# Kernel tuning notes

Measured on AMD Instinct MI355X. Metric: run time of the kernel, lower is better.

## Reference

```python
import jax, jax.numpy as jnp
import numpy as np

EPS_LN = 1e-5


def layer_norm(x, g, b):
    mu = jnp.mean(x, axis=-1, keepdims=True)
    var = jnp.mean((x - mu) ** 2, axis=-1, keepdims=True)
    return (x - mu) * jax.lax.rsqrt(var + EPS_LN) * g + b


def setup_inputs() -> dict:
    key = jax.random.key(0)
    ks = jax.random.split(key, 16)
    N, E, H, EA = 25000, 400000, 128, 1
    h = jax.random.normal(ks[0], (N, H), dtype=jnp.float32)
    coord = jax.random.normal(ks[1], (N, 3), dtype=jnp.float32)
    edge_index = jax.random.randint(ks[2], (2, E), 0, N, dtype=jnp.int64)
    edge_attr = jax.random.normal(ks[3], (E, EA), dtype=jnp.float32)

    def lin(k, fan_in, fan_out):
        lim = 1.0 / np.sqrt(fan_in)
        return jax.random.uniform(k, (fan_in, fan_out), jnp.float32, -lim, lim)

    in_edge = 2 * H + 1 + EA  # 258
    params = {
        'e_W1': lin(ks[4], in_edge, H), 'e_b1': jnp.zeros((H,), jnp.float32),
        'e_g1': jnp.ones((H,), jnp.float32), 'e_be1': jnp.zeros((H,), jnp.float32),
        'e_W2': lin(ks[5], H, H), 'e_b2': jnp.zeros((H,), jnp.float32),
        'e_g2': jnp.ones((H,), jnp.float32), 'e_be2': jnp.zeros((H,), jnp.float32),
        'n_W1': lin(ks[6], 2 * H, H), 'n_b1': jnp.zeros((H,), jnp.float32),
        'n_g1': jnp.ones((H,), jnp.float32), 'n_be1': jnp.zeros((H,), jnp.float32),
        'n_W2': lin(ks[7], H, H), 'n_b2': jnp.zeros((H,), jnp.float32),
        'c_W1': lin(ks[8], H, H), 'c_b1': jnp.zeros((H,), jnp.float32),
        'c_g1': jnp.ones((H,), jnp.float32), 'c_be1': jnp.zeros((H,), jnp.float32),
        # xavier_uniform with gain=0.001, no bias
        'c_W2': jax.random.uniform(ks[9], (H, 1), jnp.float32, -1.0, 1.0) * (0.001 * np.sqrt(6.0 / (H + 1))),
    }
    return dict(h=h, edge_index=edge_index, coord=coord, edge_attr=edge_attr, **params)


def reference(h, edge_index, coord, edge_attr,
              e_W1, e_b1, e_g1, e_be1, e_W2, e_b2, e_g2, e_be2,
              n_W1, n_b1, n_g1, n_be1, n_W2, n_b2,
              c_W1, c_b1, c_g1, c_be1, c_W2):
    N = h.shape[0]
    row, col = edge_index[0], edge_index[1]

    coord_diff = coord[row] - coord[col]                     # [E,3]
    radial = jnp.sum(coord_diff ** 2, axis=1, keepdims=True)  # [E,1]
    norm = jnp.sqrt(radial + 1e-8)
    coord_diff = coord_diff / (norm + 1.0)

    inp = jnp.concatenate([h[row], h[col], radial, edge_attr], axis=1)  # [E,258]
    x = jax.nn.silu(layer_norm(inp @ e_W1 + e_b1, e_g1, e_be1))
    edge_feat = jax.nn.silu(layer_norm(x @ e_W2 + e_b2, e_g2, e_be2))   # [E,H]

    cm = jax.nn.silu(layer_norm(edge_feat @ c_W1 + c_b1, c_g1, c_be1)) @ c_W2  # [E,1]
    trans = coord_diff * cm                                   # [E,3]

    coord_out = coord + jax.ops.segment_sum(trans, row, num_segments=N)
    agg = jax.ops.segment_sum(edge_feat, row, num_segments=N)  # [N,H]

    node_in = jnp.concatenate([h, agg], axis=1)               # [N,2H]
    out = jax.nn.silu(layer_norm(node_in @ n_W1 + n_b1, n_g1, n_be1)) @ n_W2 + n_b2
    out = h + out  # recurrent
    return out, coord_out
```

## Files before the change

### kernel.cpp

```cpp
#include <hip/hip_runtime.h>
#include <math.h>

#define H 128
#define KE 256
#define KN 256
#define XSTR 136

typedef __attribute__((ext_vector_type(8))) short bf16x8;
typedef __attribute__((ext_vector_type(4))) float f32x4;

__device__ __forceinline__ float silu_f(float x) { return x / (1.0f + __expf(-x)); }

__device__ __forceinline__ unsigned short f2bf(float f) {
    unsigned int u = __float_as_uint(f);
    unsigned int r = u + 0x7FFFu + ((u >> 16) & 1u);
    return (unsigned short)(r >> 16);
}

__device__ __forceinline__ unsigned int pkbf(float a, float b) {
#if defined(__has_builtin)
#if __has_builtin(__builtin_amdgcn_cvt_pk_bf16_f32)
    typedef __attribute__((ext_vector_type(2))) __bf16 bf16x2_t;
    bf16x2_t v = __builtin_amdgcn_cvt_pk_bf16_f32(a, b);
    return *(unsigned int*)&v;
#else
    return (unsigned int)f2bf(a) | ((unsigned int)f2bf(b) << 16);
#endif
#else
    return (unsigned int)f2bf(a) | ((unsigned int)f2bf(b) << 16);
#endif
}

__device__ __forceinline__ void atomic_pk_add_bf16(unsigned short* addr, unsigned int pkv) {
    asm volatile("global_atomic_pk_add_bf16 %0, %1, off"
                 :: "v"(addr), "v"(pkv) : "memory");
}

template<int CTRL>
__device__ __forceinline__ float dpp_add(float x) {
    int t = __builtin_amdgcn_update_dpp(0, __float_as_int(x), CTRL, 0xF, 0xF, true);
    return x + __int_as_float(t);
}
__device__ __forceinline__ float red16(float x) {
    x = dpp_add<0x128>(x);
    x = dpp_add<0x124>(x);
    x = dpp_add<0x122>(x);
    x = dpp_add<0x121>(x);
    return x;
}

__device__ __forceinline__ void wfrag(const float* __restrict__ W,
                                      unsigned short* __restrict__ Wf, int f) {
    int kb = f >> 9, rem = f & 511;
    int nt = rem >> 6, lane = rem & 63;
    int quad = lane >> 4, l15 = lane & 15;
    int n = nt * 16 + l15, k0 = kb * 32 + quad * 8;
    union { bf16x8 v; unsigned short u[8]; } pk;
    #pragma unroll
    for (int j = 0; j < 8; ++j) pk.u[j] = f2bf(W[(size_t)(k0 + j) * H + n]);
    *(bf16x8*)&Wf[(size_t)f * 8] = pk.v;
}

__global__ __launch_bounds__(256) void prep_all(
    const float* __restrict__ h, unsigned short* __restrict__ hb, int n4_h,
    float* __restrict__ aggz, int n4_agg,
    const float* __restrict__ coord, float* __restrict__ coord_out, int n_coord,
    const float* __restrict__ eW1, const float* __restrict__ eW2,
    const float* __restrict__ cW1, const float* __restrict__ nW1,
    const float* __restrict__ nW2,
    unsigned short* __restrict__ eW1f, unsigned short* __restrict__ eW2f,
    unsigned short* __restrict__ cW1f, unsigned short* __restrict__ nW1f,
    unsigned short* __restrict__ nW2f,
    int b0, int b1, int b2)
{
    int b = blockIdx.x;
    int t = threadIdx.x;
    if (b < b0) {
        int i = b * 256 + t;
        if (i < n4_h) {
            float4 f = ((const float4*)h)[i];
            ((uint2*)hb)[i] = make_uint2(pkbf(f.x, f.y), pkbf(f.z, f.w));
        }
    } else if (b < b1) {
        int i = (b - b0) * 256 + t;
        if (i < n4_agg) ((float4*)aggz)[i] = (float4){0.f, 0.f, 0.f, 0.f};
    } else if (b < b2) {
        int i = (b - b1) * 256 + t;
        if (i < n_coord) coord_out[i] = coord[i];
    } else {
        int idx = (b - b2) * 256 + t;
        if      (idx <  4096) wfrag(eW1, eW1f, idx);
        else if (idx <  8192) wfrag(nW1, nW1f, idx - 4096);
        else if (idx < 10240) wfrag(eW2, eW2f, idx - 8192);
        else if (idx < 12288) wfrag(cW1, cW1f, idx - 10240);
        else if (idx < 14336) wfrag(nW2, nW2f, idx - 12288);
    }
}

__device__ __forceinline__ void ln_silu_store1(
    f32x4* acc, const float* __restrict__ bias, const float* __restrict__ g,
    const float* __restrict__ be, unsigned short* X, int l15, int quad)
{
    float s[4] = {0,0,0,0}, q[4] = {0,0,0,0};
    #pragma unroll
    for (int nt = 0; nt < 8; ++nt) {
        float b = bias[nt * 16 + l15];
        #pragma unroll
        for (int r = 0; r < 4; ++r) {
            float x = acc[nt][r] + b; acc[nt][r] = x; s[r] += x; q[r] += x * x;
        }
    }
    #pragma unroll
    for (int r = 0; r < 4; ++r) { s[r] = red16(s[r]); q[r] = red16(q[r]); }
    #pragma unroll
    for (int r = 0; r < 4; ++r) {
        float mu = s[r] * 0.0078125f, v = q[r] * 0.0078125f - mu * mu;
        s[r] = mu; q[r] = rsqrtf(v + 1e-5f);
    }
    #pragma unroll
    for (int nt = 0; nt < 8; ++nt) {
        float gg = g[nt * 16 + l15], bb = be[nt * 16 + l15];
        float y0 = silu_f(fmaf(acc[nt][0], q[0] * gg, bb - s[0] * (q[0] * gg)));
        float y1 = silu_f(fmaf(acc[nt][1], q[1] * gg, bb - s[1] * (q[1] * gg)));
        float y2 = silu_f(fmaf(acc[nt][2], q[2] * gg, bb - s[2] * (q[2] * gg)));
        float y3 = silu_f(fmaf(acc[nt][3], q[3] * gg, bb - s[3] * (q[3] * gg)));
        acc[nt][0] = y0; acc[nt][1] = y1; acc[nt][2] = y2; acc[nt][3] = y3;
        unsigned int p01 = pkbf(y0, y1), p23 = pkbf(y2, y3);
        const int col = nt * 16 + l15;
        X[(quad * 4 + 0) * XSTR + col] = (unsigned short)p01;
        X[(quad * 4 + 1) * XSTR + col] = (unsigned short)(p01 >> 16);
        X[(quad * 4 + 2) * XSTR + col] = (unsigned short)p23;
        X[(quad * 4 + 3) * XSTR + col] = (unsigned short)(p23 >> 16);
    }
}

__global__ __launch_bounds__(64, 4) void edge_kernel(
    const unsigned short* __restrict__ hb, const int* __restrict__ ei,
    const float* __restrict__ coord, const float* __restrict__ eattr,
    const unsigned short* __restrict__ eW1f, const float* __restrict__ eW1,
    const float* __restrict__ eb1, const float* __restrict__ eg1, const float* __restrict__ ebe1,
    const unsigned short* __restrict__ eW2f,
    const float* __restrict__ eb2, const float* __restrict__ eg2, const float* __restrict__ ebe2,
    const unsigned short* __restrict__ cW1f,
    const float* __restrict__ cb1, const float* __restrict__ cg1, const float* __restrict__ cbe1,
    const float* __restrict__ cW2,
    unsigned short* __restrict__ aggb, float* __restrict__ coord_out, int E)
{
    __shared__ unsigned short X[16 * XSTR];

    const int lane = threadIdx.x;
    const int l15 = lane & 15, quad = lane >> 4;
    const int ge0 = blockIdx.x * 16;

    int el  = ge0 + l15;
    int elc = (el < E) ? el : (E - 1);
    int rowl = ei[elc], coll = ei[E + elc];
    float dx = coord[rowl * 3 + 0] - coord[coll * 3 + 0];
    float dy = coord[rowl * 3 + 1] - coord[coll * 3 + 1];
    float dz = coord[rowl * 3 + 2] - coord[coll * 3 + 2];
    float radial = dx * dx + dy * dy + dz * dz;
    float inv = 1.0f / (sqrtf(radial + 1e-8f) + 1.0f);
    float cdx = dx * inv, cdy = dy * inv, cdz = dz * inv;
    float ea = eattr[elc];

    f32x4 acc[8];
    #pragma unroll
    for (int nt = 0; nt < 8; ++nt) acc[nt] = (f32x4){0.f, 0.f, 0.f, 0.f};

    for (int kb = 0; kb < 8; ++kb) {
        int ko = (kb & 3) * 32 + quad * 8;
        bf16x8 af = *(const bf16x8*)(hb + (size_t)((kb < 4) ? rowl : coll) * H + ko);
        const unsigned short* bp = eW1f + ((size_t)kb * 8) * 512 + (size_t)lane * 8;
        #pragma unroll
        for (int nt = 0; nt < 8; ++nt) {
            bf16x8 bf = *(const bf16x8*)(bp + (size_t)nt * 512);
            acc[nt] = __builtin_amdgcn_mfma_f32_16x16x32_bf16(af, bf, acc[nt], 0, 0, 0);
        }
    }

    {
        float rad_r[4], ea_r[4];
        #pragma unroll
        for (int r = 0; r < 4; ++r) {
            rad_r[r] = __shfl(radial, quad * 4 + r, 64);
            ea_r[r]  = __shfl(ea,     quad * 4 + r, 64);
        }
        #pragma unroll
        for (int nt = 0; nt < 8; ++nt) {
            float w256 = eW1[256 * H + nt * 16 + l15];
            float w257 = eW1[257 * H + nt * 16 + l15];
            #pragma unroll
            for (int r = 0; r < 4; ++r)
                acc[nt][r] += rad_r[r] * w256 + ea_r[r] * w257;
        }
    }

    ln_silu_store1(acc, eb1, eg1, ebe1, X, l15, quad);

    f32x4 ac2[8];
    #pragma unroll
    for (int nt = 0; nt < 8; ++nt) ac2[nt] = (f32x4){0.f, 0.f, 0.f, 0.f};
    for (int kb = 0; kb < 4; ++kb) {
        bf16x8 af = *(const bf16x8*)&X[l15 * XSTR + kb * 32 + quad * 8];
        const unsigned short* bp = eW2f + ((size_t)kb * 8) * 512 + (size_t)lane * 8;
        #pragma unroll
        for (int nt = 0; nt < 8; ++nt) {
            bf16x8 bf = *(const bf16x8*)(bp + (size_t)nt * 512);
            ac2[nt] = __builtin_amdgcn_mfma_f32_16x16x32_bf16(af, bf, ac2[nt], 0, 0, 0);
        }
    }

    ln_silu_store1(ac2, eb2, eg2, ebe2, X, l15, quad);

    {
        int rowm[4];
        #pragma unroll
        for (int r = 0; r < 4; ++r) rowm[r] = __shfl(rowl, quad * 4 + r, 64);
        #pragma unroll
        for (int c4 = 0; c4 < 4; ++c4) {
            #pragma unroll
            for (int r = 0; r < 4; ++r) {
                int geh = ge0 + quad * 4 + r;
                if (geh < E) {
                    unsigned int pkv =
                        *(const unsigned int*)&X[(quad * 4 + r) * XSTR + c4 * 32 + 2 * l15];
                    atomic_pk_add_bf16(aggb + (size_t)rowm[r] * H + c4 * 32 + 2 * l15, pkv);
                }
            }
        }
    }

    #pragma unroll
    for (int nt = 0; nt < 8; ++nt) acc[nt] = (f32x4){0.f, 0.f, 0.f, 0.f};
    for (int kb = 0; kb < 4; ++kb) {
        bf16x8 af = *(const bf16x8*)&X[l15 * XSTR + kb * 32 + quad * 8];
        const unsigned short* bp = cW1f + ((size_t)kb * 8) * 512 + (size_t)lane * 8;
        #pragma unroll
        for (int nt = 0; nt < 8; ++nt) {
            bf16x8 bf = *(const bf16x8*)(bp + (size_t)nt * 512);
            acc[nt] = __builtin_amdgcn_mfma_f32_16x16x32_bf16(af, bf, acc[nt], 0, 0, 0);
        }
    }

    {
        float s[4] = {0,0,0,0}, q[4] = {0,0,0,0};
        #pragma unroll
        for (int nt = 0; nt < 8; ++nt) {
            float b = cb1[nt * 16 + l15];
            #pragma unroll
            for (int r = 0; r < 4; ++r) {
                float x = acc[nt][r] + b; acc[nt][r] = x; s[r] += x; q[r] += x * x;
            }
        }
        #pragma unroll
        for (int r = 0; r < 4; ++r) { s[r] = red16(s[r]); q[r] = red16(q[r]); }
        #pragma unroll
        for (int r = 0; r < 4; ++r) {
            float mu = s[r] * 0.0078125f, v = q[r] * 0.0078125f - mu * mu;
            s[r] = mu; q[r] = rsqrtf(v + 1e-5f);
        }
        float cm[4] = {0,0,0,0};
        #pragma unroll
        for (int nt = 0; nt < 8; ++nt) {
            float gg = cg1[nt * 16 + l15], bb = cbe1[nt * 16 + l15];
            float w2 = cW2[nt * 16 + l15];
            #pragma unroll
            for (int r = 0; r < 4; ++r) {
                float a = q[r] * gg, c = bb - s[r] * a;
                cm[r] += silu_f(acc[nt][r] * a + c) * w2;
            }
        }
        #pragma unroll
        for (int r = 0; r < 4; ++r) cm[r] = red16(cm[r]);
        #pragma unroll
        for (int r = 0; r < 4; ++r) {
            int src = quad * 4 + r;
            float cdxr = __shfl(cdx, src, 64);
            float cdyr = __shfl(cdy, src, 64);
            float cdzr = __shfl(cdz, src, 64);
            int rw = __shfl(rowl, src, 64);
            float comp = (l15 == 0) ? cdxr : ((l15 == 1) ? cdyr : cdzr);
            int geh = ge0 + src;
            if (l15 < 3 && geh < E)
                atomicAdd(&coord_out[(size_t)rw * 3 + l15], comp * cm[r]);
        }
    }
}

__global__ __launch_bounds__(256, 4) void node_kernel(
    const unsigned short* __restrict__ hb, const float* __restrict__ h,
    const unsigned short* __restrict__ aggb,
    const unsigned short* __restrict__ nW1f,
    const float* __restrict__ nb1, const float* __restrict__ ng1, const float* __restrict__ nbe1,
    const unsigned short* __restrict__ nW2f, const float* __restrict__ nb2,
    float* __restrict__ out, int N)
{
    __shared__ unsigned short Xs[4][16 * XSTR];

    const int wv   = threadIdx.x >> 6;
    const int lane = threadIdx.x & 63;
    const int l15 = lane & 15, quad = lane >> 4;
    const int gn0 = (blockIdx.x * 4 + wv) * 16;
    unsigned short* X = &Xs[wv][0];

    if (gn0 >= N) return;
    int nl = gn0 + l15; if (nl >= N) nl = N - 1;

    f32x4 acc[8];
    #pragma unroll
    for (int nt = 0; nt < 8; ++nt) acc[nt] = (f32x4){0.f, 0.f, 0.f, 0.f};

    for (int kb = 0; kb < 8; ++kb) {
        int ko = (kb & 3) * 32 + quad * 8;
        const unsigned short* src = (kb < 4) ? hb : aggb;
        bf16x8 af = *(const bf16x8*)(src + (size_t)nl * H + ko);
        const unsigned short* bp = nW1f + ((size_t)kb * 8) * 512 + (size_t)lane * 8;
        #pragma unroll
        for (int nt = 0; nt < 8; ++nt) {
            bf16x8 bf = *(const bf16x8*)(bp + (size_t)nt * 512);
            acc[nt] = __builtin_amdgcn_mfma_f32_16x16x32_bf16(af, bf, acc[nt], 0, 0, 0);
        }
    }

    ln_silu_store1(acc, nb1, ng1, nbe1, X, l15, quad);

    f32x4 ac2[8];
    #pragma unroll
    for (int nt = 0; nt < 8; ++nt) ac2[nt] = (f32x4){0.f, 0.f, 0.f, 0.f};
    for (int kb = 0; kb < 4; ++kb) {
        bf16x8 af = *(const bf16x8*)&X[l15 * XSTR + kb * 32 + quad * 8];
        const unsigned short* bp = nW2f + ((size_t)kb * 8) * 512 + (size_t)lane * 8;
        #pragma unroll
        for (int nt = 0; nt < 8; ++nt) {
            bf16x8 bf = *(const bf16x8*)(bp + (size_t)nt * 512);
            ac2[nt] = __builtin_amdgcn_mfma_f32_16x16x32_bf16(af, bf, ac2[nt], 0, 0, 0);
        }
    }

    #pragma unroll
    for (int nt = 0; nt < 8; ++nt) {
        float b = nb2[nt * 16 + l15];
        #pragma unroll
        for (int r = 0; r < 4; ++r) {
            int gn = gn0 + quad * 4 + r;
            if (gn < N) {
                size_t idx = (size_t)gn * H + nt * 16 + l15;
                out[idx] = ac2[nt][r] + b + h[idx];
            }
        }
    }
}

extern "C" void kernel_launch(void* const* d_in, const int* in_sizes, int n_in,
                              void* d_out, int out_size, void* d_ws, size_t ws_size,
                              hipStream_t stream) {
    const float* h     = (const float*)d_in[0];
    const int*   ei    = (const int*)d_in[1];
    const float* coord = (const float*)d_in[2];
    const float* eattr = (const float*)d_in[3];
    const float* eW1   = (const float*)d_in[4];
    const float* eb1   = (const float*)d_in[5];
    const float* eg1   = (const float*)d_in[6];
    const float* ebe1  = (const float*)d_in[7];
    const float* eW2   = (const float*)d_in[8];
    const float* eb2   = (const float*)d_in[9];
    const float* eg2   = (const float*)d_in[10];
    const float* ebe2  = (const float*)d_in[11];
    const float* nW1   = (const float*)d_in[12];
    const float* nb1   = (const float*)d_in[13];
    const float* ng1   = (const float*)d_in[14];
    const float* nbe1  = (const float*)d_in[15];
    const float* nW2   = (const float*)d_in[16];
    const float* nb2   = (const float*)d_in[17];
    const float* cW1   = (const float*)d_in[18];
    const float* cb1   = (const float*)d_in[19];
    const float* cg1   = (const float*)d_in[20];
    const float* cbe1  = (const float*)d_in[21];
    const float* cW2   = (const float*)d_in[22];

    const int N = in_sizes[0] / H;
    const int E = in_sizes[1] / 2;

    float* out       = (float*)d_out;
    float* coord_out = out + (size_t)N * H;

    char* ws = (char*)d_ws;
    size_t o = 0;
    unsigned short* aggb = (unsigned short*)(ws + o); o += (size_t)N * H * 2;
    unsigned short* hb   = (unsigned short*)(ws + o); o += (size_t)N * H * 2;
    unsigned short* eW1f = (unsigned short*)(ws + o); o += (size_t)H * KE * 2;
    unsigned short* eW2f = (unsigned short*)(ws + o); o += (size_t)H * H * 2;
    unsigned short* cW1f = (unsigned short*)(ws + o); o += (size_t)H * H * 2;
    unsigned short* nW1f = (unsigned short*)(ws + o); o += (size_t)H * KN * 2;
    unsigned short* nW2f = (unsigned short*)(ws + o); o += (size_t)H * H * 2;

    const int n4_h   = N * H / 4;
    const int n4_agg = N * H / 8;
    const int n_co   = N * 3;
    const int b0 = (n4_h   + 255) / 256;
    const int b1 = b0 + (n4_agg + 255) / 256;
    const int b2 = b1 + (n_co   + 255) / 256;
    const int bw = (4096 + 4096 + 2048 + 2048 + 2048 + 255) / 256;
    prep_all<<<b2 + bw, 256, 0, stream>>>(
        h, hb, n4_h, (float*)aggb, n4_agg, coord, coord_out, n_co,
        eW1, eW2, cW1, nW1, nW2,
        eW1f, eW2f, cW1f, nW1f, nW2f, b0, b1, b2);

    edge_kernel<<<(E + 15) / 16, 64, 0, stream>>>(
        hb, ei, coord, eattr,
        eW1f, eW1, eb1, eg1, ebe1,
        eW2f, eb2, eg2, ebe2,
        cW1f, cb1, cg1, cbe1, cW2,
        aggb, coord_out, E);

    node_kernel<<<(N + 63) / 64, 256, 0, stream>>>(
        hb, h, aggb, nW1f, nb1, ng1, nbe1, nW2f, nb2, out, N);
}
```

Measured before the change: 337.2 us.

## Precompute per-node edge-MLP first-layer projections and gather them per edge

The first edge linear layer is linear in h[row] and h[col], so a new kernel computes h@W1_top and h@W1_bottom once per node (N rows instead of E) and stores them as bf16. The edge kernel then gathers the two 128-wide projections per edge, sums them into shared memory and adds the radial/edge_attr terms, replacing the K=256 MFMA loop. This removes most of the first-layer FLOPs at the cost of an extra launch, an N×256 bf16 workspace and an extra bf16 rounding of the projections, which changes numerics. The per-edge gather width stays at 512 bytes, the same as before.

```diff
diff --git a/kernel.cpp b/kernel.cpp
--- a/kernel.cpp
+++ b/kernel.cpp
@@ -5,6 +5,7 @@
 #define KE 256
 #define KN 256
 #define XSTR 136
+#define SSTR 132
 
 typedef __attribute__((ext_vector_type(8))) short bf16x8;
 typedef __attribute__((ext_vector_type(4))) float f32x4;
@@ -30,6 +31,9 @@
     return (unsigned int)f2bf(a) | ((unsigned int)f2bf(b) << 16);
 #endif
 }
+
+__device__ __forceinline__ float bflo(unsigned int w) { return __uint_as_float(w << 16); }
+__device__ __forceinline__ float bfhi(unsigned int w) { return __uint_as_float(w & 0xFFFF0000u); }
 
 __device__ __forceinline__ void atomic_pk_add_bf16(unsigned short* addr, unsigned int pkv) {
     asm volatile("global_atomic_pk_add_bf16 %0, %1, off"
@@ -97,6 +101,63 @@
     }
 }
 
+__global__ __launch_bounds__(256, 4) void proj_kernel(
+    const unsigned short* __restrict__ hb,
+    const unsigned short* __restrict__ eW1f,
+    unsigned short* __restrict__ Pb, int N)
+{
+    __shared__ unsigned short Ys[4][16 * 256];
+
+    const int wv = threadIdx.x >> 6;
+    const int lane = threadIdx.x & 63;
+    const int l15 = lane & 15, quad = lane >> 4;
+    const int gn0 = (blockIdx.x * 4 + wv) * 16;
+    unsigned short* Y = &Ys[wv][0];
+
+    if (gn0 >= N) return;
+    int nl = gn0 + l15; if (nl >= N) nl = N - 1;
+
+    f32x4 a1[8], a2[8];
+    #pragma unroll
+    for (int nt = 0; nt < 8; ++nt) {
+        a1[nt] = (f32x4){0.f, 0.f, 0.f, 0.f};
+        a2[nt] = (f32x4){0.f, 0.f, 0.f, 0.f};
+    }
+
+    for (int kb = 0; kb < 4; ++kb) {
+        int ko = kb * 32 + quad * 8;
+        bf16x8 af = *(const bf16x8*)(hb + (size_t)nl * H + ko);
+        const unsigned short* bp1 = eW1f + ((size_t)kb * 8) * 512 + (size_t)lane * 8;
+        const unsigned short* bp2 = eW1f + ((size_t)(kb + 4) * 8) * 512 + (size_t)lane * 8;
+        #pragma unroll
+        for (int nt = 0; nt < 8; ++nt) {
+            bf16x8 b1 = *(const bf16x8*)(bp1 + (size_t)nt * 512);
+            bf16x8 b2 = *(const bf16x8*)(bp2 + (size_t)nt * 512);
+            a1[nt] = __builtin_amdgcn_mfma_f32_16x16x32_bf16(af, b1, a1[nt], 0, 0, 0);
+            a2[nt] = __builtin_amdgcn_mfma_f32_16x16x32_bf16(af, b2, a2[nt], 0, 0, 0);
+        }
+    }
+
+    #pragma unroll
+    for (int nt = 0; nt < 8; ++nt) {
+        int c = nt * 16 + l15;
+        #pragma unroll
+        for (int r = 0; r < 4; ++r) {
+            int rr = quad * 4 + r;
+            Y[rr * 256 + c]       = f2bf(a1[nt][r]);
+            Y[rr * 256 + 128 + c] = f2bf(a2[nt][r]);
+        }
+    }
+
+    const int m = lane >> 2, part = lane & 3;
+    int gm = gn0 + m; if (gm >= N) gm = N - 1;
+    #pragma unroll
+    for (int j = 0; j < 8; ++j) {
+        uint4 v = *(const uint4*)&Y[m * 256 + part * 64 + j * 8];
+        *(uint4*)(Pb + (size_t)gm * 256 + part * 64 + j * 8) = v;
+    }
+}
+
 __device__ __forceinline__ void ln_silu_store1(
     f32x4* acc, const float* __restrict__ bias, const float* __restrict__ g,
     const float* __restrict__ be, unsigned short* X, int l15, int quad)
@@ -120,24 +181,20 @@
     #pragma unroll
     for (int nt = 0; nt < 8; ++nt) {
         float gg = g[nt * 16 + l15], bb = be[nt * 16 + l15];
-        float y0 = silu_f(fmaf(acc[nt][0], q[0] * gg, bb - s[0] * (q[0] * gg)));
-        float y1 = silu_f(fmaf(acc[nt][1], q[1] * gg, bb - s[1] * (q[1] * gg)));
-        float y2 = silu_f(fmaf(acc[nt][2], q[2] * gg, bb - s[2] * (q[2] * gg)));
-        float y3 = silu_f(fmaf(acc[nt][3], q[3] * gg, bb - s[3] * (q[3] * gg)));
-        acc[nt][0] = y0; acc[nt][1] = y1; acc[nt][2] = y2; acc[nt][3] = y3;
-        unsigned int p01 = pkbf(y0, y1), p23 = pkbf(y2, y3);
-        const int col = nt * 16 + l15;
-        X[(quad * 4 + 0) * XSTR + col] = (unsigned short)p01;
-        X[(quad * 4 + 1) * XSTR + col] = (unsigned short)(p01 >> 16);
-        X[(quad * 4 + 2) * XSTR + col] = (unsigned short)p23;
-        X[(quad * 4 + 3) * XSTR + col] = (unsigned short)(p23 >> 16);
+        #pragma unroll
+        for (int r = 0; r < 4; ++r) {
+            float a = q[r] * gg, c = bb - s[r] * a;
+            float y = silu_f(fmaf(acc[nt][r], a, c));
+            acc[nt][r] = y;
+            X[(quad * 4 + r) * XSTR + nt * 16 + l15] = f2bf(y);
+        }
     }
 }
 
 __global__ __launch_bounds__(64, 4) void edge_kernel(
-    const unsigned short* __restrict__ hb, const int* __restrict__ ei,
+    const unsigned short* __restrict__ Pb, const int* __restrict__ ei,
     const float* __restrict__ coord, const float* __restrict__ eattr,
-    const unsigned short* __restrict__ eW1f, const float* __restrict__ eW1,
+    const float* __restrict__ eW1,
     const float* __restrict__ eb1, const float* __restrict__ eg1, const float* __restrict__ ebe1,
     const unsigned short* __restrict__ eW2f,
     const float* __restrict__ eb2, const float* __restrict__ eg2, const float* __restrict__ ebe2,
@@ -146,7 +203,8 @@
     const float* __restrict__ cW2,
     unsigned short* __restrict__ aggb, float* __restrict__ coord_out, int E)
 {
-    __shared__ unsigned short X[16 * XSTR];
+    __shared__ float S[16 * SSTR];
+    unsigned short* X = (unsigned short*)S;
 
     const int lane = threadIdx.x;
     const int l15 = lane & 15, quad = lane >> 4;
@@ -163,21 +221,27 @@
     float cdx = dx * inv, cdy = dy * inv, cdz = dz * inv;
     float ea = eattr[elc];
 
+    {
+        const int m = lane >> 2, part = lane & 3;
+        int row_m = __shfl(rowl, m, 64);
+        int col_m = __shfl(coll, m, 64);
+        const unsigned short* p1 = Pb + (size_t)row_m * 256 + part * 32;
+        const unsigned short* p2 = Pb + (size_t)col_m * 256 + 128 + part * 32;
+        #pragma unroll
+        for (int j = 0; j < 4; ++j) {
+            uint4 a = *(const uint4*)(p1 + j * 8);
+            uint4 b = *(const uint4*)(p2 + j * 8);
+            float4 v0, v1;
+            v0.x = bflo(a.x) + bflo(b.x); v0.y = bfhi(a.x) + bfhi(b.x);
+            v0.z = bflo(a.y) + bflo(b.y); v0.w = bfhi(a.y) + bfhi(b.y);
+            v1.x = bflo(a.z) + bflo(b.z); v1.y = bfhi(a.z) + bfhi(b.z);
+            v1.z = bflo(a.w) + bflo(b.w); v1.w = bfhi(a.w) + bfhi(b.w);
+            *(float4*)&S[m * SSTR + part * 32 + j * 8]     = v0;
+            *(float4*)&S[m * SSTR + part * 32 + j * 8 + 4] = v1;
+        }
+    }
+
     f32x4 acc[8];
-    #pragma unroll
-    for (int nt = 0; nt < 8; ++nt) acc[nt] = (f32x4){0.f, 0.f, 0.f, 0.f};
-
-    for (int kb = 0; kb < 8; ++kb) {
-        int ko = (kb & 3) * 32 + quad * 8;
-        bf16x8 af = *(const bf16x8*)(hb + (size_t)((kb < 4) ? rowl : coll) * H + ko);
-        const unsigned short* bp = eW1f + ((size_t)kb * 8) * 512 + (size_t)lane * 8;
-        #pragma unroll
-        for (int nt = 0; nt < 8; ++nt) {
-            bf16x8 bf = *(const bf16x8*)(bp + (size_t)nt * 512);
-            acc[nt] = __builtin_amdgcn_mfma_f32_16x16x32_bf16(af, bf, acc[nt], 0, 0, 0);
-        }
-    }
-
     {
         float rad_r[4], ea_r[4];
         #pragma unroll
@@ -190,8 +254,10 @@
             float w256 = eW1[256 * H + nt * 16 + l15];
             float w257 = eW1[257 * H + nt * 16 + l15];
             #pragma unroll
-            for (int r = 0; r < 4; ++r)
-                acc[nt][r] += rad_r[r] * w256 + ea_r[r] * w257;
+            for (int r = 0; r < 4; ++r) {
+                float base = S[(quad * 4 + r) * SSTR + nt * 16 + l15];
+                acc[nt][r] = base + rad_r[r] * w256 + ea_r[r] * w257;
+            }
         }
     }
 
@@ -267,7 +333,7 @@
             #pragma unroll
             for (int r = 0; r < 4; ++r) {
                 float a = q[r] * gg, c = bb - s[r] * a;
-                cm[r] += silu_f(acc[nt][r] * a + c) * w2;
+                cm[r] += silu_f(fmaf(acc[nt][r], a, c)) * w2;
             }
         }
         #pragma unroll
@@ -388,6 +454,7 @@
     size_t o = 0;
     unsigned short* aggb = (unsigned short*)(ws + o); o += (size_t)N * H * 2;
     unsigned short* hb   = (unsigned short*)(ws + o); o += (size_t)N * H * 2;
+    unsigned short* Pb   = (unsigned short*)(ws + o); o += (size_t)N * 256 * 2;
     unsigned short* eW1f = (unsigned short*)(ws + o); o += (size_t)H * KE * 2;
     unsigned short* eW2f = (unsigned short*)(ws + o); o += (size_t)H * H * 2;
     unsigned short* cW1f = (unsigned short*)(ws + o); o += (size_t)H * H * 2;
@@ -406,9 +473,11 @@
         eW1, eW2, cW1, nW1, nW2,
         eW1f, eW2f, cW1f, nW1f, nW2f, b0, b1, b2);
 
+    proj_kernel<<<(N + 63) / 64, 256, 0, stream>>>(hb, eW1f, Pb, N);
+
     edge_kernel<<<(E + 15) / 16, 64, 0, stream>>>(
-        hb, ei, coord, eattr,
-        eW1f, eW1, eb1, eg1, ebe1,
+        Pb, ei, coord, eattr,
+        eW1, eb1, eg1, ebe1,
         eW2f, eb2, eg2, ebe2,
         cW1f, cb1, cg1, cbe1, cW2,
         aggb, coord_out, E);
```

New measurement: 319.3 us (median of 2 runs). 1.06x faster.
